# Optimization experiments

Hardware: AMD Instinct MI355X
Metric: run time of the kernel (lower is better)

Reference implementation:

```python
import jax, jax.numpy as jnp
import numpy as np

RMS_EPS = 1e-6
COMMIT = 0.25


def rmsnorm(x, g):
    return x * jax.lax.rsqrt(jnp.mean(x * x, axis=-1, keepdims=True) + RMS_EPS) * g


def mse(a, b):
    return jnp.mean((a - b) ** 2)


def setup_inputs() -> dict:
    key = jax.random.key(0)
    ks = jax.random.split(key, 16)
    B, D_IN = 16384, 768
    HD = [512, 256, 128]
    Q, K = 4, 8192

    def lin(k, i, o):
        return jax.random.normal(k, (i, o), jnp.float32) * (1.0 / np.sqrt(i))

    inp = {
        "x": jax.random.normal(ks[0], (B, D_IN), jnp.float32),
        "emb_mean": jnp.zeros((D_IN,), jnp.float32),
        "emb_std": jnp.ones((D_IN,), jnp.float32),
        # encoder: Linear -> ReLU -> RMSNorm, three stages
        "enc_w0": lin(ks[1], D_IN, HD[0]), "enc_b0": jnp.zeros((HD[0],), jnp.float32), "enc_g0": jnp.ones((HD[0],), jnp.float32),
        "enc_w1": lin(ks[2], HD[0], HD[1]), "enc_b1": jnp.zeros((HD[1],), jnp.float32), "enc_g1": jnp.ones((HD[1],), jnp.float32),
        "enc_w2": lin(ks[3], HD[1], HD[2]), "enc_b2": jnp.zeros((HD[2],), jnp.float32), "enc_g2": jnp.ones((HD[2],), jnp.float32),
        # residual quantizer codebooks: [num_quantizers, codebook_size, embed_dim]
        "codebooks": jax.random.normal(ks[4], (Q, K, HD[2]), jnp.float32) * (1.0 / np.sqrt(HD[2])),
        # decoder: Linear -> ReLU -> RMSNorm (x2), then final Linear
        "dec_w0": lin(ks[5], HD[2], HD[1]), "dec_b0": jnp.zeros((HD[1],), jnp.float32), "dec_g0": jnp.ones((HD[1],), jnp.float32),
        "dec_w1": lin(ks[6], HD[1], HD[0]), "dec_b1": jnp.zeros((HD[0],), jnp.float32), "dec_g1": jnp.ones((HD[0],), jnp.float32),
        "dec_w2": lin(ks[7], HD[0], D_IN), "dec_b2": jnp.zeros((D_IN,), jnp.float32),
    }
    return inp


def reference(x, emb_mean, emb_std,
              enc_w0, enc_b0, enc_g0, enc_w1, enc_b1, enc_g1, enc_w2, enc_b2, enc_g2,
              codebooks,
              dec_w0, dec_b0, dec_g0, dec_w1, dec_b1, dec_g1, dec_w2, dec_b2):
    xn = (x - emb_mean) / emb_std  # normalize

    # encoder
    h = xn
    for w, b, g in ((enc_w0, enc_b0, enc_g0), (enc_w1, enc_b1, enc_g1), (enc_w2, enc_b2, enc_g2)):
        h = rmsnorm(jax.nn.relu(h @ w + b), g)

    # residual vector quantization (eval path: hard argmin + one-hot gather)
    residual = h
    quantized_sum = jnp.zeros_like(h)
    vq_loss = jnp.float32(0.0)
    ids = []
    num_q = codebooks.shape[0]
    for q in range(num_q):
        E = codebooks[q]  # [K, D]
        # squared euclidean distances [B, K]
        d = (jnp.sum(residual * residual, axis=1, keepdims=True)
             + jnp.sum(E * E, axis=1)
             - 2.0 * residual @ E.T)
        idx = jnp.argmin(d, axis=1)          # [B]
        quantized = E[idx]                   # gather, [B, D]
        e_lat = mse(residual, jax.lax.stop_gradient(quantized))
        q_lat = mse(quantized, jax.lax.stop_gradient(residual))
        vq_loss = vq_loss + q_lat + COMMIT * e_lat
        # straight-through estimator
        quantized_st = residual + jax.lax.stop_gradient(quantized - residual)
        quantized_sum = quantized_sum + quantized_st
        residual = residual - jax.lax.stop_gradient(quantized)
        ids.append(idx)

    # decoder
    y = quantized_sum
    for w, b, g in ((dec_w0, dec_b0, dec_g0), (dec_w1, dec_b1, dec_g1)):
        y = rmsnorm(jax.nn.relu(y @ w + b), g)
    reconstructed = y @ dec_w2 + dec_b2

    recon_loss = mse(reconstructed, xn)
    semantic_ids = jnp.stack(ids, axis=1)  # [B, num_quantizers]
    return reconstructed, semantic_ids, recon_loss, vq_loss
```

## Files before the change

### kernel.cpp

```cpp
#include <hip/hip_runtime.h>
#include <math.h>

#define NB 16384
#define DIN 768

typedef _Float16 f16x8 __attribute__((ext_vector_type(8)));
typedef float f32x16 __attribute__((ext_vector_type(16)));


__global__ void k_zero2(float* a, float* b) {
    if (threadIdx.x == 0) { *a = 0.f; *b = 0.f; }
}

__global__ void k_norm(const float* __restrict__ x, const float* __restrict__ m,
                       const float* __restrict__ s, float* __restrict__ xn) {
    int i = blockIdx.x * 256 + threadIdx.x;
    int j = i % DIN;
    xn[i] = (x[i] - m[j]) / s[j];
}

__global__ void k_cbnorm(const float* __restrict__ cb, float* __restrict__ cbn) {
    int row = blockIdx.x * 4 + (threadIdx.x >> 6);
    int lane = threadIdx.x & 63;
    const float* p = cb + (size_t)row * 128;
    float v0 = p[lane], v1 = p[lane + 64];
    float s = v0 * v0 + v1 * v1;
    #pragma unroll
    for (int m = 32; m >= 1; m >>= 1) s += __shfl_xor(s, m, 64);
    if (lane == 0) cbn[row] = s * 4096.f;
}

__global__ void k_split(const float* __restrict__ src, _Float16* __restrict__ dst,
                        float scale) {
    int i = blockIdx.x * 256 + threadIdx.x;
    int row = i >> 7, d = i & 127;
    float v = src[i] * scale;
    _Float16 hi = (_Float16)v;
    dst[(size_t)row * 256 + d] = hi;
    dst[(size_t)row * 256 + 128 + d] = (_Float16)(v - (float)hi);
}

__global__ void k_esplit(const float* __restrict__ cb, _Float16* __restrict__ Esp) {
    int i = blockIdx.x * 256 + threadIdx.x;
    int q = i >> 20;
    int rem = i & 1048575;
    int c = rem >> 7, k = rem & 127;
    float v = cb[i] * 256.f;
    _Float16 hi = (_Float16)v;
    _Float16 lo = (_Float16)(v - (float)hi);
    int sh = k >> 3, j = k & 7;
    size_t base = (size_t)q * 2097152 + (size_t)(c >> 5) * 8192 + (size_t)(c & 31) * 8 + j;
    Esp[base + (size_t)sh * 256] = hi;
    Esp[base + (size_t)(16 + sh) * 256] = lo;
}

__global__ void k_wsplit(const float* __restrict__ W, _Float16* __restrict__ Wt,
                         int K, int N) {
    int i = blockIdx.x * 256 + threadIdx.x;
    int k = i / N, c = i - k * N;
    float v = W[i] * 256.f;
    _Float16 hi = (_Float16)v;
    _Float16 lo = (_Float16)(v - (float)hi);
    int kc = k >> 5, kin = k & 31;
    int t = kin >> 4, gg = (kin >> 3) & 1, j = kin & 7;
    size_t base = ((size_t)(kc * 8) * N + c) * 8 + j;
    Wt[base + (size_t)(t * 2 + gg) * N * 8] = hi;
    Wt[base + (size_t)(4 + t * 2 + gg) * N * 8] = lo;
}

template <int N>
__global__ __launch_bounds__(512, 2) void k_mfma_rms(
    const float* __restrict__ A, const _Float16* __restrict__ Wt,
    const float* __restrict__ bias, const float* __restrict__ g,
    float* __restrict__ out, int K) {
    constexpr int CT = N / 128;
    __shared__ __align__(16) _Float16 Bs[2][N * 64];
    __shared__ float ssbuf[64][4];
    const int tid = threadIdx.x;
    const int w = tid >> 6, lane = tid & 63;
    const int wr = w >> 2, wc = w & 3;
    const int g32 = lane >> 5, cl = lane & 31;
    const int row0 = blockIdx.x * 64;
    const int NC = K >> 5;

    const float* ap = A + (size_t)(row0 + wr * 32 + cl) * K + g32 * 8;

    f32x16 acc[CT];
    #pragma unroll
    for (int tt = 0; tt < CT; tt++)
        #pragma unroll
        for (int m = 0; m < 16; m++) acc[tt][m] = 0.f;

    float4 Ar0[4], Ar1[4];

    auto STAGE = [&](int ch, int b) {
        const _Float16* gp = Wt + (size_t)ch * 8 * N * 8;
        #pragma unroll
        for (int p = 0; p < N / 64; p++) {
            int f = tid + 512 * p;
            __builtin_amdgcn_global_load_lds(
                (const __attribute__((address_space(1))) void*)(gp + (size_t)f * 8),
                (__attribute__((address_space(3))) void*)(&Bs[b][(size_t)f * 8]),
                16, 0, 0);
        }
    };
    auto AISSUE = [&](int ch, float4* Ar) {
        const float* bsrc = ap + ch * 32;
        Ar[0] = *(const float4*)(bsrc);
        Ar[1] = *(const float4*)(bsrc + 4);
        Ar[2] = *(const float4*)(bsrc + 16);
        Ar[3] = *(const float4*)(bsrc + 20);
    };
    auto COMPUTE = [&](int b, const float4* Ar) {
        #pragma unroll
        for (int t = 0; t < 2; t++) {
            float vv[8] = {Ar[t * 2].x, Ar[t * 2].y, Ar[t * 2].z, Ar[t * 2].w,
                           Ar[t * 2 + 1].x, Ar[t * 2 + 1].y, Ar[t * 2 + 1].z, Ar[t * 2 + 1].w};
            f16x8 ah, al;
            #pragma unroll
            for (int j = 0; j < 8; j++) {
                float v = vv[j] * 16.f;
                _Float16 h = (_Float16)v;
                ah[j] = h;
                al[j] = (_Float16)(v - (float)h);
            }
            f16x8 bh[CT], bl[CT];
            #pragma unroll
            for (int tt = 0; tt < CT; tt++) {
                int c = wc * (N / 4) + tt * 32 + cl;
                bh[tt] = *(const f16x8*)&Bs[b][((size_t)(t * 2 + g32) * N + c) * 8];
                bl[tt] = *(const f16x8*)&Bs[b][((size_t)(4 + t * 2 + g32) * N + c) * 8];
            }
            #pragma unroll
            for (int tt = 0; tt < CT; tt++)
                acc[tt] = __builtin_amdgcn_mfma_f32_32x32x16_f16(ah, bh[tt], acc[tt], 0, 0, 0);
            #pragma unroll
            for (int tt = 0; tt < CT; tt++)
                acc[tt] = __builtin_amdgcn_mfma_f32_32x32x16_f16(al, bh[tt], acc[tt], 0, 0, 0);
            #pragma unroll
            for (int tt = 0; tt < CT; tt++)
                acc[tt] = __builtin_amdgcn_mfma_f32_32x32x16_f16(ah, bl[tt], acc[tt], 0, 0, 0);
        }
    };

    AISSUE(0, Ar0);
    STAGE(0, 0);
    for (int ch = 0; ch < NC; ch += 2) {
        __syncthreads();
        STAGE(ch + 1, 1);
        AISSUE(ch + 1, Ar1);
        COMPUTE(0, Ar0);
        __syncthreads();
        if (ch + 2 < NC) { STAGE(ch + 2, 0); AISSUE(ch + 2, Ar0); }
        COMPUTE(1, Ar1);
    }

    constexpr float INV = 1.f / 4096.f;
    float bb[CT], gv[CT];
    #pragma unroll
    for (int tt = 0; tt < CT; tt++) {
        int c = wc * (N / 4) + tt * 32 + cl;
        bb[tt] = bias[c];
        gv[tt] = g[c];
    }
    float ssm[16];
    #pragma unroll
    for (int m = 0; m < 16; m++) ssm[m] = 0.f;
    #pragma unroll
    for (int tt = 0; tt < CT; tt++)
        #pragma unroll
        for (int m = 0; m < 16; m++) {
            float v = fmaf(acc[tt][m], INV, bb[tt]);
            v = v > 0.f ? v : 0.f;
            acc[tt][m] = v;
            ssm[m] = fmaf(v, v, ssm[m]);
        }
    #pragma unroll
    for (int mask = 1; mask < 32; mask <<= 1)
        #pragma unroll
        for (int m = 0; m < 16; m++) ssm[m] += __shfl_xor(ssm[m], mask, 64);
    if (cl == 0) {
        #pragma unroll
        for (int m = 0; m < 16; m++) {
            int rl = wr * 32 + (m & 3) + 8 * (m >> 2) + 4 * g32;
            ssbuf[rl][wc] = ssm[m];
        }
    }
    __syncthreads();
    #pragma unroll
    for (int m = 0; m < 16; m++) {
        int rl = wr * 32 + (m & 3) + 8 * (m >> 2) + 4 * g32;
        float s4 = (ssbuf[rl][0] + ssbuf[rl][1]) + (ssbuf[rl][2] + ssbuf[rl][3]);
        float sc = 1.0f / sqrtf(s4 * (1.0f / (float)N) + 1e-6f);
        #pragma unroll
        for (int tt = 0; tt < CT; tt++) {
            int c = wc * (N / 4) + tt * 32 + cl;
            out[(size_t)(row0 + rl) * N + c] = acc[tt][m] * sc * gv[tt];
        }
    }
}

__global__ __launch_bounds__(512, 2) void k_mfma_dec2(
    const float* __restrict__ A, const _Float16* __restrict__ Wt,
    const float* __restrict__ bias, float* __restrict__ rec,
    float* __restrict__ loss_acc, int K) {
    constexpr int NT = 256, NF = 768, CT = 2;
    __shared__ __align__(16) _Float16 Bs[2][NT * 64];
    __shared__ float red[8];
    const int tid = threadIdx.x;
    const int w = tid >> 6, lane = tid & 63;
    const int wr = w >> 2, wc = w & 3;
    const int g32 = lane >> 5, cl = lane & 31;
    const int row0 = blockIdx.x * 64;
    const int col0 = blockIdx.y * NT;
    const int NC = K >> 5;

    const float* ap = A + (size_t)(row0 + wr * 32 + cl) * K + g32 * 8;

    f32x16 acc[CT];
    #pragma unroll
    for (int tt = 0; tt < CT; tt++)
        #pragma unroll
        for (int m = 0; m < 16; m++) acc[tt][m] = 0.f;

    float4 Ar0[4], Ar1[4];

    auto STAGE = [&](int ch, int b) {
        #pragma unroll
        for (int p = 0; p < 4; p++) {
            int f = tid + 512 * p;
            int s = f >> 8, cloc = f & 255;
            const _Float16* gp = Wt + ((size_t)(ch * 8 + s) * NF + col0 + cloc) * 8;
            __builtin_amdgcn_global_load_lds(
                (const __attribute__((address_space(1))) void*)gp,
                (__attribute__((address_space(3))) void*)(&Bs[b][(size_t)f * 8]),
                16, 0, 0);
        }
    };
    auto AISSUE = [&](int ch, float4* Ar) {
        const float* bsrc = ap + ch * 32;
        Ar[0] = *(const float4*)(bsrc);
        Ar[1] = *(const float4*)(bsrc + 4);
        Ar[2] = *(const float4*)(bsrc + 16);
        Ar[3] = *(const float4*)(bsrc + 20);
    };
    auto COMPUTE = [&](int b, const float4* Ar) {
        #pragma unroll
        for (int t = 0; t < 2; t++) {
            float vv[8] = {Ar[t * 2].x, Ar[t * 2].y, Ar[t * 2].z, Ar[t * 2].w,
                           Ar[t * 2 + 1].x, Ar[t * 2 + 1].y, Ar[t * 2 + 1].z, Ar[t * 2 + 1].w};
            f16x8 ah, al;
            #pragma unroll
            for (int j = 0; j < 8; j++) {
                float v = vv[j] * 16.f;
                _Float16 h = (_Float16)v;
                ah[j] = h;
                al[j] = (_Float16)(v - (float)h);
            }
            f16x8 bh[CT], bl[CT];
            #pragma unroll
            for (int tt = 0; tt < CT; tt++) {
                int c = wc * 64 + tt * 32 + cl;
                bh[tt] = *(const f16x8*)&Bs[b][((size_t)(t * 2 + g32) * NT + c) * 8];
                bl[tt] = *(const f16x8*)&Bs[b][((size_t)(4 + t * 2 + g32) * NT + c) * 8];
            }
            #pragma unroll
            for (int tt = 0; tt < CT; tt++)
                acc[tt] = __builtin_amdgcn_mfma_f32_32x32x16_f16(ah, bh[tt], acc[tt], 0, 0, 0);
            #pragma unroll
            for (int tt = 0; tt < CT; tt++)
                acc[tt] = __builtin_amdgcn_mfma_f32_32x32x16_f16(al, bh[tt], acc[tt], 0, 0, 0);
            #pragma unroll
            for (int tt = 0; tt < CT; tt++)
                acc[tt] = __builtin_amdgcn_mfma_f32_32x32x16_f16(ah, bl[tt], acc[tt], 0, 0, 0);
        }
    };

    AISSUE(0, Ar0);
    STAGE(0, 0);
    for (int ch = 0; ch < NC; ch += 2) {
        __syncthreads();
        STAGE(ch + 1, 1);
        AISSUE(ch + 1, Ar1);
        COMPUTE(0, Ar0);
        __syncthreads();
        if (ch + 2 < NC) { STAGE(ch + 2, 0); AISSUE(ch + 2, Ar0); }
        COMPUTE(1, Ar1);
    }

    constexpr float INV = 1.f / 4096.f;
    float lsum = 0.f;
    #pragma unroll
    for (int tt = 0; tt < CT; tt++) {
        int cg = col0 + wc * 64 + tt * 32 + cl;
        float bb = bias[cg];
        #pragma unroll
        for (int m = 0; m < 16; m++) {
            int rl = wr * 32 + (m & 3) + 8 * (m >> 2) + 4 * g32;
            float v = fmaf(acc[tt][m], INV, bb);
            size_t o = (size_t)(row0 + rl) * NF + cg;
            float e = v - rec[o];
            lsum = fmaf(e, e, lsum);
            rec[o] = v;
        }
    }
    #pragma unroll
    for (int mask = 1; mask < 64; mask <<= 1) lsum += __shfl_xor(lsum, mask, 64);
    if (lane == 0) red[w] = lsum;
    __syncthreads();
    if (tid == 0) {
        float t = 0.f;
        #pragma unroll
        for (int i = 0; i < 8; i++) t += red[i];
        atomicAdd(loss_acc, t * (1.0f / ((float)NB * (float)DIN)));
    }
}

__global__ __launch_bounds__(256, 2) void k_vq_argmin_mfma(
    const _Float16* __restrict__ Rsp, const _Float16* __restrict__ Esp,
    const float* __restrict__ cbnS,
    float* __restrict__ pbest, int* __restrict__ pidx) {
    __shared__ __align__(16) _Float16 Es[2][8192];
    const int tid = threadIdx.x;
    const int w = tid >> 6, lane = tid & 63;
    const int g = lane >> 5, cl31 = lane & 31;
    const int rt0 = blockIdx.x * 256 + w * 64;
    const int cbase = blockIdx.y * 512;
    const int ch0 = blockIdx.y * 16;

    f16x8 Rh0[8], Rl0[8], Rh1[8], Rl1[8];
    {
        const _Float16* rp0 = Rsp + (size_t)(rt0 + cl31) * 256 + g * 8;
        const _Float16* rp1 = rp0 + 32 * 256;
        #pragma unroll
        for (int kc = 0; kc < 8; kc++) {
            Rh0[kc] = *(const f16x8*)(rp0 + kc * 16);
            Rl0[kc] = *(const f16x8*)(rp0 + 128 + kc * 16);
            Rh1[kc] = *(const f16x8*)(rp1 + kc * 16);
            Rl1[kc] = *(const f16x8*)(rp1 + 128 + kc * 16);
        }
    }

    f32x16 zz;
    #pragma unroll
    for (int m = 0; m < 16; m++) zz[m] = 0.f;

    float best0 = 3.402823466e+38f, best1 = 3.402823466e+38f;
    int bidx0 = 0, bidx1 = 0;

    auto STAGE = [&](int gch, int b) {
        const _Float16* gp = Esp + (size_t)gch * 8192;
        #pragma unroll
        for (int p = 0; p < 4; p++) {
            int f = tid + 256 * p;
            __builtin_amdgcn_global_load_lds(
                (const __attribute__((address_space(1))) void*)(gp + (size_t)f * 8),
                (__attribute__((address_space(3))) void*)(&Es[b][(size_t)f * 8]),
                16, 0, 0);
        }
    };

    STAGE(ch0, 0);
    for (int ch = 0; ch < 16; ch++) {
        const int buf = ch & 1;
        const int c0c = cbase + ch * 32;
        f32x16 cv;
        #pragma unroll
        for (int q = 0; q < 4; q++) {
            float4 v = *(const float4*)(cbnS + c0c + q * 8 + 4 * g);
            cv[q * 4 + 0] = v.x; cv[q * 4 + 1] = v.y;
            cv[q * 4 + 2] = v.z; cv[q * 4 + 3] = v.w;
        }
        __syncthreads();
        if (ch < 15) STAGE(ch0 + ch + 1, buf ^ 1);
        f32x16 c0, c1, c2, c3, c4, c5;
        __builtin_amdgcn_s_setprio(1);
        {
            f16x8 eh = *(const f16x8*)&Es[buf][g * 256 + cl31 * 8];
            f16x8 el = *(const f16x8*)&Es[buf][(16 + g) * 256 + cl31 * 8];
            c0 = __builtin_amdgcn_mfma_f32_32x32x16_f16(eh, Rh0[0], cv, 0, 0, 0);
            c3 = __builtin_amdgcn_mfma_f32_32x32x16_f16(eh, Rh1[0], cv, 0, 0, 0);
            c1 = __builtin_amdgcn_mfma_f32_32x32x16_f16(el, Rh0[0], zz, 0, 0, 0);
            c4 = __builtin_amdgcn_mfma_f32_32x32x16_f16(el, Rh1[0], zz, 0, 0, 0);
            c2 = __builtin_amdgcn_mfma_f32_32x32x16_f16(eh, Rl0[0], zz, 0, 0, 0);
            c5 = __builtin_amdgcn_mfma_f32_32x32x16_f16(eh, Rl1[0], zz, 0, 0, 0);
        }
        #pragma unroll
        for (int kc = 1; kc < 8; kc++) {
            int sh = kc * 2 + g;
            f16x8 eh = *(const f16x8*)&Es[buf][sh * 256 + cl31 * 8];
            f16x8 el = *(const f16x8*)&Es[buf][(16 + sh) * 256 + cl31 * 8];
            c0 = __builtin_amdgcn_mfma_f32_32x32x16_f16(eh, Rh0[kc], c0, 0, 0, 0);
            c3 = __builtin_amdgcn_mfma_f32_32x32x16_f16(eh, Rh1[kc], c3, 0, 0, 0);
            c1 = __builtin_amdgcn_mfma_f32_32x32x16_f16(el, Rh0[kc], c1, 0, 0, 0);
            c4 = __builtin_amdgcn_mfma_f32_32x32x16_f16(el, Rh1[kc], c4, 0, 0, 0);
            c2 = __builtin_amdgcn_mfma_f32_32x32x16_f16(eh, Rl0[kc], c2, 0, 0, 0);
            c5 = __builtin_amdgcn_mfma_f32_32x32x16_f16(eh, Rl1[kc], c5, 0, 0, 0);
        }
        __builtin_amdgcn_s_setprio(0);
        const int c0g = c0c + 4 * g;
        #pragma unroll
        for (int m = 0; m < 16; m++) {
            int c = c0g + ((m & 3) + 8 * (m >> 2));
            float s0 = (c0[m] + c1[m]) + c2[m];
            float s1 = (c3[m] + c4[m]) + c5[m];
            if (s0 < best0) { best0 = s0; bidx0 = c; }
            if (s1 < best1) { best1 = s1; bidx1 = c; }
        }
    }

    {
        float ob = __shfl_xor(best0, 32, 64);
        int oi = __shfl_xor(bidx0, 32, 64);
        if (ob < best0 || (ob == best0 && oi < bidx0)) { best0 = ob; bidx0 = oi; }
        ob = __shfl_xor(best1, 32, 64);
        oi = __shfl_xor(bidx1, 32, 64);
        if (ob < best1 || (ob == best1 && oi < bidx1)) { best1 = ob; bidx1 = oi; }
    }
    if (lane < 32) {
        const int part = blockIdx.y;
        pbest[(size_t)part * NB + rt0 + cl31] = best0;
        pidx [(size_t)part * NB + rt0 + cl31] = bidx0;
        pbest[(size_t)part * NB + rt0 + 32 + cl31] = best1;
        pidx [(size_t)part * NB + rt0 + 32 + cl31] = bidx1;
    }
}

__global__ void k_vq_reduce(const float* __restrict__ pbest, const int* __restrict__ pidx,
                            int* __restrict__ idx_out, float* __restrict__ ids_f) {
    int row = blockIdx.x * 256 + threadIdx.x;
    float b = pbest[row];
    int bi = pidx[row];
    #pragma unroll
    for (int s = 1; s < 16; s++) {
        float ob = pbest[(size_t)s * NB + row];
        int oi = pidx[(size_t)s * NB + row];
        if (ob < b || (ob == b && oi < bi)) { b = ob; bi = oi; }
    }
    idx_out[row] = bi;
    ids_f[(size_t)row * 4] = (float)bi;
}

__global__ void k_vq_update(const float* __restrict__ Rin, const int* __restrict__ idx,
                            const float* __restrict__ E, float* __restrict__ Rout,
                            float* __restrict__ qsum, float* __restrict__ part,
                            int firstq, _Float16* __restrict__ Rsp) {
    __shared__ float ps[4];
    int t = blockIdx.x * 256 + threadIdx.x;
    int i0 = t * 8;
    int row = i0 >> 7, d0 = i0 & 127;
    const float* ep = E + (size_t)idx[row] * 128 + d0;
    float4 e0 = *(const float4*)ep, e1 = *(const float4*)(ep + 4);
    float4 r0 = *(const float4*)&Rin[i0], r1 = *(const float4*)&Rin[i0 + 4];
    float rv[8] = {r0.x - e0.x, r0.y - e0.y, r0.z - e0.z, r0.w - e0.w,
                   r1.x - e1.x, r1.y - e1.y, r1.z - e1.z, r1.w - e1.w};
    *(float4*)&Rout[i0]     = make_float4(rv[0], rv[1], rv[2], rv[3]);
    *(float4*)&Rout[i0 + 4] = make_float4(rv[4], rv[5], rv[6], rv[7]);
    if (firstq) {
        *(float4*)&qsum[i0] = e0;
        *(float4*)&qsum[i0 + 4] = e1;
    } else {
        float4 q0 = *(const float4*)&qsum[i0], q1 = *(const float4*)&qsum[i0 + 4];
        *(float4*)&qsum[i0]     = make_float4(q0.x + e0.x, q0.y + e0.y, q0.z + e0.z, q0.w + e0.w);
        *(float4*)&qsum[i0 + 4] = make_float4(q1.x + e1.x, q1.y + e1.y, q1.z + e1.z, q1.w + e1.w);
    }
    f16x8 hi, lo;
    float p = 0.f;
    #pragma unroll
    for (int j = 0; j < 8; j++) {
        float rs = rv[j] * -32.f;
        _Float16 h = (_Float16)rs;
        hi[j] = h;
        lo[j] = (_Float16)(rs - (float)h);
        p = fmaf(rv[j], rv[j], p);
    }
    *(f16x8*)&Rsp[(size_t)row * 256 + d0] = hi;
    *(f16x8*)&Rsp[(size_t)row * 256 + 128 + d0] = lo;
    #pragma unroll
    for (int m = 1; m < 64; m <<= 1) p += __shfl_xor(p, m, 64);
    int lane = threadIdx.x & 63, wv = threadIdx.x >> 6;
    if (lane == 0) ps[wv] = p;
    __syncthreads();
    if (threadIdx.x == 0)
        part[blockIdx.x] = (ps[0] + ps[1]) + (ps[2] + ps[3]);
}

__global__ void k_vq_acc(const float* __restrict__ part, float* __restrict__ vl) {
    __shared__ float ps[4];
    float s = 0.f;
    for (int i = threadIdx.x; i < 4096; i += 256) s += part[i];
    #pragma unroll
    for (int m = 1; m < 64; m <<= 1) s += __shfl_xor(s, m, 64);
    int lane = threadIdx.x & 63, wv = threadIdx.x >> 6;
    if (lane == 0) ps[wv] = s;
    __syncthreads();
    if (threadIdx.x == 0)
        *vl = ((ps[0] + ps[1]) + (ps[2] + ps[3])) * (1.25f / ((float)NB * 128.f));
}


extern "C" void kernel_launch(void* const* d_in, const int* in_sizes, int n_in,
                              void* d_out, int out_size, void* d_ws, size_t ws_size,
                              hipStream_t stream) {
    (void)in_sizes; (void)n_in; (void)out_size; (void)ws_size;
    const float* x        = (const float*)d_in[0];
    const float* emb_mean = (const float*)d_in[1];
    const float* emb_std  = (const float*)d_in[2];
    const float* enc_w0 = (const float*)d_in[3];
    const float* enc_b0 = (const float*)d_in[4];
    const float* enc_g0 = (const float*)d_in[5];
    const float* enc_w1 = (const float*)d_in[6];
    const float* enc_b1 = (const float*)d_in[7];
    const float* enc_g1 = (const float*)d_in[8];
    const float* enc_w2 = (const float*)d_in[9];
    const float* enc_b2 = (const float*)d_in[10];
    const float* enc_g2 = (const float*)d_in[11];
    const float* cb     = (const float*)d_in[12];
    const float* dec_w0 = (const float*)d_in[13];
    const float* dec_b0 = (const float*)d_in[14];
    const float* dec_g0 = (const float*)d_in[15];
    const float* dec_w1 = (const float*)d_in[16];
    const float* dec_b1 = (const float*)d_in[17];
    const float* dec_g1 = (const float*)d_in[18];
    const float* dec_w2 = (const float*)d_in[19];
    const float* dec_b2 = (const float*)d_in[20];

    float* out   = (float*)d_out;
    float* xn    = out;
    float* ids_f = out + (size_t)NB * DIN;
    float* rl    = out + (size_t)NB * DIN + (size_t)NB * 4;
    float* vl    = rl + 1;

    float* ws   = (float*)d_ws;
    float* h0   = ws;
    float* h1   = h0 + (size_t)NB * 512;
    float* h2   = h1 + (size_t)NB * 256;
    float* rbuf = h2 + (size_t)NB * 128;
    float* qsum = rbuf + (size_t)NB * 128;
    float* cbn  = qsum + (size_t)NB * 128;
    int*   idxb = (int*)(cbn + 4 * 8192);
    float* vqp  = (float*)(idxb + NB);

    float*    pbest = h0;
    int*      pidx  = (int*)(h0 + 16 * (size_t)NB);
    _Float16* Rsp   = (_Float16*)(h0 + 32 * (size_t)NB);
    _Float16* Esp   = (_Float16*)(h0 + 32 * (size_t)NB + (size_t)NB * 128);

    _Float16* WtE0 = (_Float16*)rbuf;
    _Float16* WtE1 = WtE0 + 786432;
    _Float16* WtE2 = WtE0 + 1048576;
    _Float16* WtD0 = (_Float16*)rbuf;
    _Float16* WtD1 = WtD0 + 65536;
    _Float16* WtD2 = WtD0 + 327680;

    k_zero2<<<1, 64, 0, stream>>>(rl, vl);
    k_norm<<<(NB * DIN) / 256, 256, 0, stream>>>(x, emb_mean, emb_std, xn);
    k_cbnorm<<<(4 * 8192) / 4, 256, 0, stream>>>(cb, cbn);

    k_wsplit<<<(768 * 512) / 256, 256, 0, stream>>>(enc_w0, WtE0, 768, 512);
    k_wsplit<<<(512 * 256) / 256, 256, 0, stream>>>(enc_w1, WtE1, 512, 256);
    k_wsplit<<<(256 * 128) / 256, 256, 0, stream>>>(enc_w2, WtE2, 256, 128);

    k_mfma_rms<512><<<NB / 64, 512, 0, stream>>>(xn, WtE0, enc_b0, enc_g0, h0, 768);
    k_mfma_rms<256><<<NB / 64, 512, 0, stream>>>(h0, WtE1, enc_b1, enc_g1, h1, 512);
    k_mfma_rms<128><<<NB / 64, 512, 0, stream>>>(h1, WtE2, enc_b2, enc_g2, h2, 256);

    k_esplit<<<(4 * 8192 * 128) / 256, 256, 0, stream>>>(cb, Esp);
    k_split<<<(NB * 128) / 256, 256, 0, stream>>>(h2, Rsp, -32.f);

    for (int q = 0; q < 4; q++) {
        const float* R = (q == 0) ? h2 : rbuf;
        const float* Eq = cb + (size_t)q * 8192 * 128;
        const _Float16* EspQ = Esp + (size_t)q * 2097152;
        dim3 gq(NB / 256, 16);
        k_vq_argmin_mfma<<<gq, 256, 0, stream>>>(Rsp, EspQ, cbn + q * 8192, pbest, pidx);
        k_vq_reduce<<<NB / 256, 256, 0, stream>>>(pbest, pidx, idxb, ids_f + q);
        k_vq_update<<<(NB * 128) / 2048, 256, 0, stream>>>(R, idxb, Eq, rbuf, qsum,
                                                           vqp + q * 1024, q == 0 ? 1 : 0, Rsp);
    }
    k_vq_acc<<<1, 256, 0, stream>>>(vqp, vl);

    k_wsplit<<<(128 * 256) / 256, 256, 0, stream>>>(dec_w0, WtD0, 128, 256);
    k_wsplit<<<(256 * 512) / 256, 256, 0, stream>>>(dec_w1, WtD1, 256, 512);
    k_wsplit<<<(512 * 768) / 256, 256, 0, stream>>>(dec_w2, WtD2, 512, 768);

    k_mfma_rms<256><<<NB / 64, 512, 0, stream>>>(qsum, WtD0, dec_b0, dec_g0, h1, 128);
    k_mfma_rms<512><<<NB / 64, 512, 0, stream>>>(h1, WtD1, dec_b1, dec_g1, h0, 256);

    dim3 g2(NB / 64, 3);
    k_mfma_dec2<<<g2, 512, 0, stream>>>(h0, WtD2, dec_b2, xn, rl, 512);
}
```

Measured before the change: 913.3 us.

## Stage 64-code chunks in VQ argmin and reduce accumulator count

Result: faster. 874.6 us (-4.2%).

```diff
diff --git a/kernel.cpp b/kernel.cpp
--- a/kernel.cpp
+++ b/kernel.cpp
@@ -49,9 +49,9 @@
     _Float16 hi = (_Float16)v;
     _Float16 lo = (_Float16)(v - (float)hi);
     int sh = k >> 3, j = k & 7;
-    size_t base = (size_t)q * 2097152 + (size_t)(c >> 5) * 8192 + (size_t)(c & 31) * 8 + j;
-    Esp[base + (size_t)sh * 256] = hi;
-    Esp[base + (size_t)(16 + sh) * 256] = lo;
+    size_t base = (size_t)q * 2097152 + (size_t)(c >> 6) * 16384 + (size_t)(c & 63) * 8 + j;
+    Esp[base + (size_t)sh * 512] = hi;
+    Esp[base + (size_t)(16 + sh) * 512] = lo;
 }
 
 __global__ void k_wsplit(const float* __restrict__ W, _Float16* __restrict__ Wt,
@@ -320,13 +320,13 @@
     const _Float16* __restrict__ Rsp, const _Float16* __restrict__ Esp,
     const float* __restrict__ cbnS,
     float* __restrict__ pbest, int* __restrict__ pidx) {
-    __shared__ __align__(16) _Float16 Es[2][8192];
+    __shared__ __align__(16) _Float16 Es[2][16384];
     const int tid = threadIdx.x;
     const int w = tid >> 6, lane = tid & 63;
     const int g = lane >> 5, cl31 = lane & 31;
     const int rt0 = blockIdx.x * 256 + w * 64;
     const int cbase = blockIdx.y * 512;
-    const int ch0 = blockIdx.y * 16;
+    const int ch0 = blockIdx.y * 8;
 
     f16x8 Rh0[8], Rl0[8], Rh1[8], Rl1[8];
     {
@@ -341,17 +341,13 @@
         }
     }
 
-    f32x16 zz;
-    #pragma unroll
-    for (int m = 0; m < 16; m++) zz[m] = 0.f;
-
     float best0 = 3.402823466e+38f, best1 = 3.402823466e+38f;
     int bidx0 = 0, bidx1 = 0;
 
     auto STAGE = [&](int gch, int b) {
-        const _Float16* gp = Esp + (size_t)gch * 8192;
-        #pragma unroll
-        for (int p = 0; p < 4; p++) {
+        const _Float16* gp = Esp + (size_t)gch * 16384;
+        #pragma unroll
+        for (int p = 0; p < 8; p++) {
             int f = tid + 256 * p;
             __builtin_amdgcn_global_load_lds(
                 (const __attribute__((address_space(1))) void*)(gp + (size_t)f * 8),
@@ -361,51 +357,51 @@
     };
 
     STAGE(ch0, 0);
-    for (int ch = 0; ch < 16; ch++) {
+    for (int ch = 0; ch < 8; ch++) {
         const int buf = ch & 1;
-        const int c0c = cbase + ch * 32;
-        f32x16 cv;
+        const int c0c = cbase + ch * 64;
+        float cnv0[16], cnv1[16];
         #pragma unroll
         for (int q = 0; q < 4; q++) {
-            float4 v = *(const float4*)(cbnS + c0c + q * 8 + 4 * g);
-            cv[q * 4 + 0] = v.x; cv[q * 4 + 1] = v.y;
-            cv[q * 4 + 2] = v.z; cv[q * 4 + 3] = v.w;
+            float4 v0 = *(const float4*)(cbnS + c0c + q * 8 + 4 * g);
+            float4 v1 = *(const float4*)(cbnS + c0c + 32 + q * 8 + 4 * g);
+            cnv0[q * 4 + 0] = v0.x; cnv0[q * 4 + 1] = v0.y;
+            cnv0[q * 4 + 2] = v0.z; cnv0[q * 4 + 3] = v0.w;
+            cnv1[q * 4 + 0] = v1.x; cnv1[q * 4 + 1] = v1.y;
+            cnv1[q * 4 + 2] = v1.z; cnv1[q * 4 + 3] = v1.w;
         }
         __syncthreads();
-        if (ch < 15) STAGE(ch0 + ch + 1, buf ^ 1);
-        f32x16 c0, c1, c2, c3, c4, c5;
-        __builtin_amdgcn_s_setprio(1);
-        {
-            f16x8 eh = *(const f16x8*)&Es[buf][g * 256 + cl31 * 8];
-            f16x8 el = *(const f16x8*)&Es[buf][(16 + g) * 256 + cl31 * 8];
-            c0 = __builtin_amdgcn_mfma_f32_32x32x16_f16(eh, Rh0[0], cv, 0, 0, 0);
-            c3 = __builtin_amdgcn_mfma_f32_32x32x16_f16(eh, Rh1[0], cv, 0, 0, 0);
-            c1 = __builtin_amdgcn_mfma_f32_32x32x16_f16(el, Rh0[0], zz, 0, 0, 0);
-            c4 = __builtin_amdgcn_mfma_f32_32x32x16_f16(el, Rh1[0], zz, 0, 0, 0);
-            c2 = __builtin_amdgcn_mfma_f32_32x32x16_f16(eh, Rl0[0], zz, 0, 0, 0);
-            c5 = __builtin_amdgcn_mfma_f32_32x32x16_f16(eh, Rl1[0], zz, 0, 0, 0);
-        }
-        #pragma unroll
-        for (int kc = 1; kc < 8; kc++) {
-            int sh = kc * 2 + g;
-            f16x8 eh = *(const f16x8*)&Es[buf][sh * 256 + cl31 * 8];
-            f16x8 el = *(const f16x8*)&Es[buf][(16 + sh) * 256 + cl31 * 8];
-            c0 = __builtin_amdgcn_mfma_f32_32x32x16_f16(eh, Rh0[kc], c0, 0, 0, 0);
-            c3 = __builtin_amdgcn_mfma_f32_32x32x16_f16(eh, Rh1[kc], c3, 0, 0, 0);
-            c1 = __builtin_amdgcn_mfma_f32_32x32x16_f16(el, Rh0[kc], c1, 0, 0, 0);
-            c4 = __builtin_amdgcn_mfma_f32_32x32x16_f16(el, Rh1[kc], c4, 0, 0, 0);
-            c2 = __builtin_amdgcn_mfma_f32_32x32x16_f16(eh, Rl0[kc], c2, 0, 0, 0);
-            c5 = __builtin_amdgcn_mfma_f32_32x32x16_f16(eh, Rl1[kc], c5, 0, 0, 0);
-        }
-        __builtin_amdgcn_s_setprio(0);
-        const int c0g = c0c + 4 * g;
-        #pragma unroll
-        for (int m = 0; m < 16; m++) {
-            int c = c0g + ((m & 3) + 8 * (m >> 2));
-            float s0 = (c0[m] + c1[m]) + c2[m];
-            float s1 = (c3[m] + c4[m]) + c5[m];
-            if (s0 < best0) { best0 = s0; bidx0 = c; }
-            if (s1 < best1) { best1 = s1; bidx1 = c; }
+        if (ch < 7) STAGE(ch0 + ch + 1, buf ^ 1);
+        #pragma unroll
+        for (int st = 0; st < 2; st++) {
+            const int cloc = st * 32 + cl31;
+            const float* cnv = st ? cnv1 : cnv0;
+            f32x16 c00, c01, c10, c11;
+            #pragma unroll
+            for (int m = 0; m < 16; m++) { c00[m] = 0.f; c01[m] = 0.f; c10[m] = 0.f; c11[m] = 0.f; }
+            __builtin_amdgcn_s_setprio(1);
+            #pragma unroll
+            for (int kc = 0; kc < 8; kc++) {
+                int sh = kc * 2 + g;
+                f16x8 eh = *(const f16x8*)&Es[buf][sh * 512 + cloc * 8];
+                f16x8 el = *(const f16x8*)&Es[buf][(16 + sh) * 512 + cloc * 8];
+                c00 = __builtin_amdgcn_mfma_f32_32x32x16_f16(eh, Rh0[kc], c00, 0, 0, 0);
+                c01 = __builtin_amdgcn_mfma_f32_32x32x16_f16(eh, Rh1[kc], c01, 0, 0, 0);
+                c10 = __builtin_amdgcn_mfma_f32_32x32x16_f16(eh, Rl0[kc], c10, 0, 0, 0);
+                c00 = __builtin_amdgcn_mfma_f32_32x32x16_f16(el, Rh0[kc], c00, 0, 0, 0);
+                c01 = __builtin_amdgcn_mfma_f32_32x32x16_f16(el, Rh1[kc], c01, 0, 0, 0);
+                c11 = __builtin_amdgcn_mfma_f32_32x32x16_f16(eh, Rl1[kc], c11, 0, 0, 0);
+            }
+            __builtin_amdgcn_s_setprio(0);
+            const int c0g = c0c + st * 32 + 4 * g;
+            #pragma unroll
+            for (int m = 0; m < 16; m++) {
+                int c = c0g + ((m & 3) + 8 * (m >> 2));
+                float s0 = (c00[m] + c10[m]) + cnv[m];
+                float s1 = (c01[m] + c11[m]) + cnv[m];
+                if (s0 < best0) { best0 = s0; bidx0 = c; }
+                if (s1 < best1) { best1 = s1; bidx1 = c; }
+            }
         }
     }
 
```
